# Optimization experiments

Hardware: AMD Instinct MI355X
Metric: run time of the kernel (lower is better)

The kernel has to match this reference:

```python
import jax, jax.numpy as jnp
import numpy as np

FEAT_STRIDE = 16
PRE_NMS, POST_NMS, NMS_THRESH = 6000, 300, 0.7  # state == 'test'

# ---- anchor generation (numpy, done once) ----

def _whctrs(a):
    w = a[2] - a[0] + 1.0
    h = a[3] - a[1] + 1.0
    return w, h, a[0] + 0.5 * (w - 1.0), a[1] + 0.5 * (h - 1.0)

def _mkanchors(ws, hs, xc, yc):
    return np.stack([xc - 0.5 * (ws - 1.0), yc - 0.5 * (hs - 1.0),
                     xc + 0.5 * (ws - 1.0), yc + 0.5 * (hs - 1.0)], axis=1)

def generate_anchors(base_size, scales, ratios):
    base = np.array([0.0, 0.0, base_size - 1.0, base_size - 1.0], np.float64)
    w, h, xc, yc = _whctrs(base)
    size = w * h
    ws = np.round(np.sqrt(size / ratios))
    hs = np.round(ws * ratios)
    ratio_anchors = _mkanchors(ws, hs, xc, yc)
    out = []
    for i in range(ratio_anchors.shape[0]):
        w, h, xc, yc = _whctrs(ratio_anchors[i])
        out.append(_mkanchors(w * scales, h * scales, xc, yc))
    return np.concatenate(out, 0).astype(np.float32)  # [9, 4]

# ---- box utilities ----

def bbox_transform_inv(anchors, deltas):
    widths = anchors[..., 2] - anchors[..., 0] + 1.0
    heights = anchors[..., 3] - anchors[..., 1] + 1.0
    cx = anchors[..., 0] + 0.5 * widths
    cy = anchors[..., 1] + 0.5 * heights
    dx, dy, dw, dh = deltas[..., 0], deltas[..., 1], deltas[..., 2], deltas[..., 3]
    pcx = dx * widths + cx
    pcy = dy * heights + cy
    pw = jnp.exp(dw) * widths
    ph = jnp.exp(dh) * heights
    return jnp.stack([pcx - 0.5 * pw, pcy - 0.5 * ph,
                      pcx + 0.5 * pw, pcy + 0.5 * ph], axis=-1)

def clip_boxes(boxes, img_info):
    # img_info = [height, width]
    x1 = jnp.clip(boxes[..., 0], 0.0, img_info[1] - 1.0)
    y1 = jnp.clip(boxes[..., 1], 0.0, img_info[0] - 1.0)
    x2 = jnp.clip(boxes[..., 2], 0.0, img_info[1] - 1.0)
    y2 = jnp.clip(boxes[..., 3], 0.0, img_info[0] - 1.0)
    return jnp.stack([x1, y1, x2, y2], axis=-1)

def nms_keep(boxes, thresh):
    # boxes [N,4], already sorted by score descending; returns bool keep mask [N]
    n = boxes.shape[0]
    x1, y1, x2, y2 = boxes[:, 0], boxes[:, 1], boxes[:, 2], boxes[:, 3]
    areas = (x2 - x1 + 1.0) * (y2 - y1 + 1.0)
    xx1 = jnp.maximum(x1[:, None], x1[None, :])
    yy1 = jnp.maximum(y1[:, None], y1[None, :])
    xx2 = jnp.minimum(x2[:, None], x2[None, :])
    yy2 = jnp.minimum(y2[:, None], y2[None, :])
    inter = jnp.maximum(0.0, xx2 - xx1 + 1.0) * jnp.maximum(0.0, yy2 - yy1 + 1.0)
    iou = inter / (areas[:, None] + areas[None, :] - inter)  # [N,N]
    over = iou > thresh
    idxs = jnp.arange(n)
    def step(suppressed, i):
        kept = jnp.logical_not(suppressed[i])
        suppressed = suppressed | (kept & over[i] & (idxs > i))
        return suppressed, kept
    _, keep = jax.lax.scan(step, jnp.zeros(n, bool), idxs)
    return keep


def setup_inputs() -> dict:
    key = jax.random.key(0)
    k1, k2 = jax.random.split(key)
    B, H, W = 4, 64, 64
    scores = jax.random.normal(k1, (B, 18, H, W), dtype=jnp.float32)
    bbox_deltas = jax.random.normal(k2, (B, 36, H, W), dtype=jnp.float32)
    img_info = jnp.array([H * FEAT_STRIDE, W * FEAT_STRIDE], dtype=jnp.float32)
    anchors = jnp.asarray(generate_anchors(FEAT_STRIDE,
                                           np.array([8.0, 16.0, 32.0]),
                                           np.array([0.5, 1.0, 2.0])))
    return {"scores": scores, "bbox_deltas": bbox_deltas,
            "img_info": img_info, "anchors": anchors}


def reference(scores, bbox_deltas, img_info, anchors):
    B = scores.shape[0]
    A = anchors.shape[0]
    fg = scores[:, A:]                       # [B, A, H, W] foreground scores
    H, W = fg.shape[2], fg.shape[3]
    sx = jnp.arange(W, dtype=scores.dtype) * FEAT_STRIDE
    sy = jnp.arange(H, dtype=scores.dtype) * FEAT_STRIDE
    gx, gy = jnp.meshgrid(sx, sy)            # 'xy' indexing -> [H, W]
    shifts = jnp.stack([gx.ravel(), gy.ravel(), gx.ravel(), gy.ravel()], -1)  # [K,4]
    all_anchors = (anchors[None] + shifts[:, None]).reshape(-1, 4)            # [K*A,4]
    scs = fg.transpose(0, 2, 3, 1).reshape(B, -1)                # [B, K*A]
    deltas = bbox_deltas.transpose(0, 2, 3, 1).reshape(B, -1, 4)  # [B, K*A, 4]
    props = bbox_transform_inv(all_anchors[None], deltas)
    props = clip_boxes(props, img_info)

    def per_image(args):
        p, s = args
        _, order = jax.lax.top_k(s, PRE_NMS)          # descending score order
        b = p[order]                                   # [PRE_NMS, 4]
        keep = nms_keep(b, NMS_THRESH)
        idx = jnp.where(keep, size=POST_NMS, fill_value=-1)[0]
        valid = (idx >= 0).astype(b.dtype)
        sel = b[jnp.maximum(idx, 0)] * valid[:, None]  # zero-pad missing rows
        return sel                                      # [POST_NMS, 4]

    sel = jax.lax.map(per_image, (props, scs))          # [B, POST_NMS, 4]
    bidx = jnp.broadcast_to(jnp.arange(B, dtype=sel.dtype)[:, None, None],
                            (B, POST_NMS, 1))
    return jnp.concatenate([bidx, sel], axis=-1)        # [B, POST_NMS, 5]
```

## Files before the change

### kernel.cpp

```cpp
#include <hip/hip_runtime.h>
#include <stdint.h>

#define HH 64
#define WW 64
#define AA 9
#define N_PER (HH*WW*AA)
#define NB 4
#define PRE_NMS 6000
#define POST_NMS 300
#define NMS_THRESH 0.7f
#define FEAT_STRIDE 16
#define M 1024
#define MW 16
#define BINS 8192
#define SCAT_MAX 8000

__global__ void __launch_bounds__(1024) select_rank(const float* __restrict__ scores,
                                                    const float* __restrict__ deltas,
                                                    const float* __restrict__ img_info,
                                                    const float* __restrict__ anchors,
                                                    float* __restrict__ topb)
{
#pragma clang fp contract(off)
    int b = blockIdx.x;
    int t = threadIdx.x;
    __shared__ uint32_t H[BINS];
    __shared__ uint32_t SS[BINS];
    __shared__ uint64_t scat[SCAT_MAX];
    __shared__ uint32_t blksum[1024];
    __shared__ int shB1;
    __shared__ uint32_t shNscat;

    auto keyof = [&](int j) -> uint64_t {
        int a = j >> 12, hw = j & 4095;
        float sc = scores[((size_t)b*18 + 9 + a)*4096 + hw];
        uint32_t u = __float_as_uint(sc);
        u = (u & 0x80000000u) ? ~u : (u | 0x80000000u);
        uint32_t i = (uint32_t)(hw*9 + a);
        return ((uint64_t)u << 32) | (uint32_t)(~i);
    };

    for (int i = t; i < BINS; i += 1024) H[i] = 0u;
    __syncthreads();
    for (int j = t; j < N_PER; j += 1024)
        atomicAdd(&H[(uint32_t)(keyof(j) >> 51)], 1u);
    __syncthreads();

    int base = t * 8;
    uint32_t loc[8];
    uint32_t lsum = 0;
    #pragma unroll
    for (int k = 0; k < 8; ++k) { loc[k] = H[base + k]; lsum += loc[k]; }
    blksum[t] = lsum;
    __syncthreads();
    for (int off = 1; off < 1024; off <<= 1) {
        uint32_t add = (t + off < 1024) ? blksum[t + off] : 0u;
        __syncthreads();
        blksum[t] += add;
        __syncthreads();
    }
    uint32_t run = (t < 1023) ? blksum[t + 1] : 0u;
    #pragma unroll
    for (int k = 7; k >= 0; --k) { SS[base + k] = run; run += loc[k]; }
    __syncthreads();

    for (int i = t; i < BINS; i += 1024) {
        if (SS[i] < PRE_NMS && SS[i] + H[i] >= PRE_NMS) shB1 = i;
    }
    __syncthreads();
    int B1 = shB1;
    if (t == 0) shNscat = SS[B1] + H[B1];
    __syncthreads();

    for (int j = t; j < N_PER; j += 1024) {
        uint64_t k64 = keyof(j);
        uint32_t bin = (uint32_t)(k64 >> 51);
        if ((int)bin >= B1) {
            uint32_t slot = atomicAdd(&SS[bin], 1u);
            if (slot < SCAT_MAX) scat[slot] = k64;
        }
    }
    __syncthreads();
    uint32_t Nscat = min(shNscat, (uint32_t)SCAT_MAX);

    float maxx = img_info[1] - 1.0f;
    float maxy = img_info[0] - 1.0f;
    for (uint32_t s = t; s < Nscat; s += 1024) {
        uint64_t k64 = scat[s];
        uint32_t bin = (uint32_t)(k64 >> 51);
        uint32_t end = SS[bin];
        uint32_t start = end - H[bin];
        uint32_t cnt = 0;
        for (uint32_t j = start; j < end; ++j)
            cnt += (scat[j] > k64) ? 1u : 0u;
        uint32_t r = start + cnt;
        if (r < PRE_NMS) {
            uint32_t i = ~(uint32_t)(k64 & 0xFFFFFFFFu);
            int a = (int)(i % 9u);
            int hw = (int)(i / 9u);
            int h = hw >> 6, w = hw & 63;
            float sx = (float)(w * FEAT_STRIDE);
            float sy = (float)(h * FEAT_STRIDE);
            float ax1 = anchors[a*4+0] + sx;
            float ay1 = anchors[a*4+1] + sy;
            float ax2 = anchors[a*4+2] + sx;
            float ay2 = anchors[a*4+3] + sy;
            float width  = ax2 - ax1 + 1.0f;
            float height = ay2 - ay1 + 1.0f;
            float cx = ax1 + 0.5f * width;
            float cy = ay1 + 0.5f * height;
            size_t dbase = ((size_t)b*36 + a*4) * 4096 + hw;
            float dx = deltas[dbase];
            float dy = deltas[dbase + 4096];
            float dw = deltas[dbase + 2*4096];
            float dh = deltas[dbase + 3*4096];
            float pcx = dx * width + cx;
            float pcy = dy * height + cy;
            float pw = (float)exp((double)dw) * width;
            float ph = (float)exp((double)dh) * height;
            float x1 = pcx - 0.5f * pw;
            float y1 = pcy - 0.5f * ph;
            float x2 = pcx + 0.5f * pw;
            float y2 = pcy + 0.5f * ph;
            x1 = fminf(fmaxf(x1, 0.0f), maxx);
            y1 = fminf(fmaxf(y1, 0.0f), maxy);
            x2 = fminf(fmaxf(x2, 0.0f), maxx);
            y2 = fminf(fmaxf(y2, 0.0f), maxy);
            *(float4*)(topb + ((size_t)b*PRE_NMS + r)*4) = make_float4(x1, y1, x2, y2);
        }
    }
}

__global__ void __launch_bounds__(64) nms_mask_small(const float* __restrict__ topb,
                                                     uint64_t* __restrict__ msk) {
#pragma clang fp contract(off)
    int jblock = blockIdx.x;
    int iblock = blockIdx.y;
    int b = blockIdx.z;
    int t = threadIdx.x;
    __shared__ float4 jb[64];
    __shared__ float jarea[64];
    int j0 = jblock*64;
    {
        float4 bj = *(const float4*)(topb + ((size_t)b*PRE_NMS + j0 + t)*4);
        jb[t] = bj;
        jarea[t] = (bj.z - bj.x + 1.0f) * (bj.w - bj.y + 1.0f);
    }
    __syncthreads();
    int i = iblock*64 + t;
    float4 bi = *(const float4*)(topb + ((size_t)b*PRE_NMS + i)*4);
    float areai = (bi.z - bi.x + 1.0f) * (bi.w - bi.y + 1.0f);
    uint64_t bits = 0;
    for (int jj = 0; jj < 64; ++jj) {
        float4 bj = jb[jj];
        float xx1 = fmaxf(bi.x, bj.x);
        float yy1 = fmaxf(bi.y, bj.y);
        float xx2 = fminf(bi.z, bj.z);
        float yy2 = fminf(bi.w, bj.w);
        float iw = fmaxf(0.0f, xx2 - xx1 + 1.0f);
        float ih = fmaxf(0.0f, yy2 - yy1 + 1.0f);
        float inter = iw * ih;
        float iou = inter / ((areai + jarea[jj]) - inter);
        if (iou > NMS_THRESH) bits |= (1ull << jj);
    }
    msk[((size_t)b*M + i)*MW + jblock] = bits;
}

__global__ void __launch_bounds__(64) nms_scan_lds(const uint64_t* __restrict__ msk,
                                                   const float* __restrict__ topb,
                                                   float* __restrict__ out) {
#pragma clang fp contract(off)
    int b = blockIdx.x;
    int l = threadIdx.x;
    __shared__ __align__(16) uint64_t rows[M][MW];
    __shared__ int keepL[POST_NMS];
    __shared__ float skx1[POST_NMS], sky1[POST_NMS], skx2[POST_NMS], sky2[POST_NMS], skar[POST_NMS];

    const uint8_t* src0 = (const uint8_t*)(msk + (size_t)b*M*MW);
    uint8_t* dst0 = (uint8_t*)&rows[0][0];
    for (int it = 0; it < (M*MW*8)/1024; ++it) {
        __builtin_amdgcn_global_load_lds(
            (const __attribute__((address_space(1))) uint32_t*)(src0 + it*1024 + l*16),
            (__attribute__((address_space(3))) uint32_t*)(dst0 + it*1024 + l*16),
            16, 0, 0);
    }
    asm volatile("s_waitcnt vmcnt(0)" ::: "memory");
    __builtin_amdgcn_sched_barrier(0);

    uint64_t remv = 0ull;
    int nkeep = 0;
    int cur = 0;
    bool exhausted = false;
    while (true) {
        if (l == 0) keepL[nkeep] = cur;
        nkeep++;
        if (nkeep >= POST_NMS) break;
        uint64_t rw = (l < MW) ? rows[cur][l] : 0ull;
        remv |= rw;
        uint64_t live = (l < MW) ? ~remv : 0ull;
        int local = live ? (l*64 + (int)__builtin_ctzll(live)) : 0x7FFFFFFF;
        uint64_t mb = __ballot(live != 0ull);
        if (mb == 0ull) { exhausted = true; break; }
        cur = __builtin_amdgcn_readlane(local, (int)__builtin_ctzll(mb));
    }

    if (nkeep < POST_NMS && exhausted) {
        for (int k = l; k < nkeep; k += 64) {
            float4 bx = *(const float4*)(topb + ((size_t)b*PRE_NMS + keepL[k])*4);
            skx1[k] = bx.x; sky1[k] = bx.y; skx2[k] = bx.z; sky2[k] = bx.w;
            skar[k] = (bx.z - bx.x + 1.0f) * (bx.w - bx.y + 1.0f);
        }
        int base = M;
        while (nkeep < POST_NMS && base < PRE_NMS) {
            int c = base + l;
            float4 bc = make_float4(0.f, 0.f, 0.f, 0.f);
            bool sup = true;
            if (c < PRE_NMS) {
                bc = *(const float4*)(topb + ((size_t)b*PRE_NMS + c)*4);
                sup = false;
            }
            float ac = (bc.z - bc.x + 1.0f) * (bc.w - bc.y + 1.0f);
            for (int k = 0; k < nkeep; ++k) {
                float xx1 = fmaxf(skx1[k], bc.x);
                float yy1 = fmaxf(sky1[k], bc.y);
                float xx2 = fminf(skx2[k], bc.z);
                float yy2 = fminf(sky2[k], bc.w);
                float iw = fmaxf(0.0f, xx2 - xx1 + 1.0f);
                float ih = fmaxf(0.0f, yy2 - yy1 + 1.0f);
                float inter = iw * ih;
                float iou = inter / ((skar[k] + ac) - inter);
                if (iou > NMS_THRESH) sup = true;
            }
            uint64_t live = __ballot(!sup);
            while (live != 0ull && nkeep < POST_NMS) {
                int j = (int)__builtin_ctzll(live);
                int cj = base + j;
                if (l == 0) keepL[nkeep] = cj;
                float jx1 = __shfl(bc.x, j);
                float jy1 = __shfl(bc.y, j);
                float jx2 = __shfl(bc.z, j);
                float jy2 = __shfl(bc.w, j);
                float ja  = __shfl(ac, j);
                if (l == 0) { skx1[nkeep]=jx1; sky1[nkeep]=jy1; skx2[nkeep]=jx2; sky2[nkeep]=jy2; skar[nkeep]=ja; }
                nkeep++;
                float xx1 = fmaxf(jx1, bc.x);
                float yy1 = fmaxf(jy1, bc.y);
                float xx2 = fminf(jx2, bc.z);
                float yy2 = fminf(jy2, bc.w);
                float iw = fmaxf(0.0f, xx2 - xx1 + 1.0f);
                float ih = fmaxf(0.0f, yy2 - yy1 + 1.0f);
                float inter = iw * ih;
                float iou = inter / ((ja + ac) - inter);
                uint64_t kill = __ballot(iou > NMS_THRESH);
                live &= ~kill;
                live &= ~(1ull << j);
            }
            base += 64;
        }
    }
    __syncthreads();

    for (int k = l; k < POST_NMS; k += 64) {
        float* o = out + ((size_t)b*POST_NMS + k)*5;
        o[0] = (float)b;
        if (k < nkeep) {
            float4 bx = *(const float4*)(topb + ((size_t)b*PRE_NMS + keepL[k])*4);
            o[1] = bx.x; o[2] = bx.y; o[3] = bx.z; o[4] = bx.w;
        } else {
            o[1] = 0.0f; o[2] = 0.0f; o[3] = 0.0f; o[4] = 0.0f;
        }
    }
}

extern "C" void kernel_launch(void* const* d_in, const int* in_sizes, int n_in,
                              void* d_out, int out_size, void* d_ws, size_t ws_size,
                              hipStream_t stream) {
    const float* scores   = (const float*)d_in[0];
    const float* deltas   = (const float*)d_in[1];
    const float* img_info = (const float*)d_in[2];
    const float* anchors  = (const float*)d_in[3];
    float* out = (float*)d_out;

    uint8_t* ws = (uint8_t*)d_ws;
    float*    topb = (float*)ws;
    uint64_t* msk  = (uint64_t*)(ws + 393216);

    select_rank<<<NB, 1024, 0, stream>>>(scores, deltas, img_info, anchors, topb);

    dim3 mg(MW, MW, NB);
    nms_mask_small<<<mg, 64, 0, stream>>>(topb, msk);

    nms_scan_lds<<<NB, 64, 0, stream>>>(msk, topb, out);
}
```

Measured before the change: 202.4 us.

## Split per-image select/rank kernel into grid-wide histogram, scan, scatter and rank kernels

The single-block-per-image select_rank kernel is replaced by four kernels: a grid-wide global-atomic histogram, a per-image prefix scan and cutoff search, a grid-wide scatter of candidate keys, and a multi-block rank-and-decode pass. The intent is to spread the 36864-element-per-image work across many CUs instead of only four blocks. The cost is extra launches, a memset, global atomics in place of LDS atomics, and intermediates stored in global workspace rather than shared memory.

```diff
diff --git a/kernel.cpp b/kernel.cpp
--- a/kernel.cpp
+++ b/kernel.cpp
@@ -15,42 +15,49 @@
 #define BINS 8192
 #define SCAT_MAX 8000
 
-__global__ void __launch_bounds__(1024) select_rank(const float* __restrict__ scores,
-                                                    const float* __restrict__ deltas,
-                                                    const float* __restrict__ img_info,
-                                                    const float* __restrict__ anchors,
-                                                    float* __restrict__ topb)
-{
-#pragma clang fp contract(off)
+#define OFF_TOPB   0u
+#define OFF_MSK    393216u
+#define OFF_H      917504u
+#define OFF_SS     1048576u
+#define OFF_CUR    1179648u
+#define OFF_B1     1310720u
+#define OFF_NSEL   1310736u
+#define OFF_SCAT   1310752u
+
+__device__ __forceinline__ uint64_t make_key(const float* __restrict__ scores, int b, int j) {
+    int a = j >> 12, hw = j & 4095;
+    float sc = scores[((size_t)b*18 + 9 + a)*4096 + hw];
+    uint32_t u = __float_as_uint(sc);
+    u = (u & 0x80000000u) ? ~u : (u | 0x80000000u);
+    uint32_t i = (uint32_t)(hw*9 + a);
+    return ((uint64_t)u << 32) | (uint32_t)(~i);
+}
+
+__global__ void __launch_bounds__(1024) hist_kernel(const float* __restrict__ scores,
+                                                    uint32_t* __restrict__ Hg) {
+    int tid = blockIdx.x*1024 + threadIdx.x;
+    int b = tid / N_PER;
+    int j = tid - b*N_PER;
+    uint64_t k64 = make_key(scores, b, j);
+    atomicAdd(&Hg[(uint32_t)b*BINS + (uint32_t)(k64 >> 51)], 1u);
+}
+
+__global__ void __launch_bounds__(1024) scan_cutoff(const uint32_t* __restrict__ Hg,
+                                                    uint32_t* __restrict__ SSg,
+                                                    uint32_t* __restrict__ CURg,
+                                                    uint32_t* __restrict__ B1g,
+                                                    uint32_t* __restrict__ NselG) {
     int b = blockIdx.x;
     int t = threadIdx.x;
-    __shared__ uint32_t H[BINS];
     __shared__ uint32_t SS[BINS];
-    __shared__ uint64_t scat[SCAT_MAX];
     __shared__ uint32_t blksum[1024];
     __shared__ int shB1;
-    __shared__ uint32_t shNscat;
-
-    auto keyof = [&](int j) -> uint64_t {
-        int a = j >> 12, hw = j & 4095;
-        float sc = scores[((size_t)b*18 + 9 + a)*4096 + hw];
-        uint32_t u = __float_as_uint(sc);
-        u = (u & 0x80000000u) ? ~u : (u | 0x80000000u);
-        uint32_t i = (uint32_t)(hw*9 + a);
-        return ((uint64_t)u << 32) | (uint32_t)(~i);
-    };
-
-    for (int i = t; i < BINS; i += 1024) H[i] = 0u;
-    __syncthreads();
-    for (int j = t; j < N_PER; j += 1024)
-        atomicAdd(&H[(uint32_t)(keyof(j) >> 51)], 1u);
-    __syncthreads();
 
     int base = t * 8;
     uint32_t loc[8];
     uint32_t lsum = 0;
     #pragma unroll
-    for (int k = 0; k < 8; ++k) { loc[k] = H[base + k]; lsum += loc[k]; }
+    for (int k = 0; k < 8; ++k) { loc[k] = Hg[(uint32_t)b*BINS + base + k]; lsum += loc[k]; }
     blksum[t] = lsum;
     __syncthreads();
     for (int off = 1; off < 1024; off <<= 1) {
@@ -63,72 +70,94 @@
     #pragma unroll
     for (int k = 7; k >= 0; --k) { SS[base + k] = run; run += loc[k]; }
     __syncthreads();
-
-    for (int i = t; i < BINS; i += 1024) {
-        if (SS[i] < PRE_NMS && SS[i] + H[i] >= PRE_NMS) shB1 = i;
-    }
-    __syncthreads();
-    int B1 = shB1;
-    if (t == 0) shNscat = SS[B1] + H[B1];
-    __syncthreads();
-
-    for (int j = t; j < N_PER; j += 1024) {
-        uint64_t k64 = keyof(j);
-        uint32_t bin = (uint32_t)(k64 >> 51);
-        if ((int)bin >= B1) {
-            uint32_t slot = atomicAdd(&SS[bin], 1u);
-            if (slot < SCAT_MAX) scat[slot] = k64;
-        }
-    }
-    __syncthreads();
-    uint32_t Nscat = min(shNscat, (uint32_t)SCAT_MAX);
-
+    #pragma unroll
+    for (int k = 0; k < 8; ++k) {
+        if (SS[base + k] < PRE_NMS && SS[base + k] + loc[k] >= PRE_NMS) shB1 = base + k;
+    }
+    __syncthreads();
+    #pragma unroll
+    for (int k = 0; k < 8; ++k) {
+        SSg[(uint32_t)b*BINS + base + k]  = SS[base + k];
+        CURg[(uint32_t)b*BINS + base + k] = SS[base + k];
+    }
+    if (t == 0) {
+        B1g[b] = (uint32_t)shB1;
+        NselG[b] = SS[shB1] + Hg[(uint32_t)b*BINS + shB1];
+    }
+}
+
+__global__ void __launch_bounds__(1024) scatter_kernel(const float* __restrict__ scores,
+                                                       const uint32_t* __restrict__ B1g,
+                                                       uint32_t* __restrict__ CURg,
+                                                       uint64_t* __restrict__ scatG) {
+    int tid = blockIdx.x*1024 + threadIdx.x;
+    int b = tid / N_PER;
+    int j = tid - b*N_PER;
+    uint64_t k64 = make_key(scores, b, j);
+    uint32_t bin = (uint32_t)(k64 >> 51);
+    if (bin >= B1g[b]) {
+        uint32_t slot = atomicAdd(&CURg[(uint32_t)b*BINS + bin], 1u);
+        if (slot < SCAT_MAX) scatG[(uint32_t)b*SCAT_MAX + slot] = k64;
+    }
+}
+
+__global__ void __launch_bounds__(1024) rank_decode(const uint64_t* __restrict__ scatG,
+                                                    const uint32_t* __restrict__ SSg,
+                                                    const uint32_t* __restrict__ CURg,
+                                                    const uint32_t* __restrict__ NselG,
+                                                    const float* __restrict__ deltas,
+                                                    const float* __restrict__ img_info,
+                                                    const float* __restrict__ anchors,
+                                                    float* __restrict__ topb) {
+#pragma clang fp contract(off)
+    int b = blockIdx.y;
+    uint32_t s = blockIdx.x*1024u + threadIdx.x;
+    uint32_t n = min(NselG[b], (uint32_t)SCAT_MAX);
+    if (s >= n) return;
+    uint64_t k64 = scatG[(uint32_t)b*SCAT_MAX + s];
+    uint32_t bin = (uint32_t)(k64 >> 51);
+    uint32_t start = SSg[(uint32_t)b*BINS + bin];
+    uint32_t end = min(CURg[(uint32_t)b*BINS + bin], (uint32_t)SCAT_MAX);
+    uint32_t cnt = 0;
+    for (uint32_t j = start; j < end; ++j)
+        cnt += (scatG[(uint32_t)b*SCAT_MAX + j] > k64) ? 1u : 0u;
+    uint32_t r = start + cnt;
+    if (r >= PRE_NMS) return;
+
+    uint32_t i = ~(uint32_t)(k64 & 0xFFFFFFFFu);
+    int a = (int)(i % 9u);
+    int hw = (int)(i / 9u);
+    int h = hw >> 6, w = hw & 63;
+    float sx = (float)(w * FEAT_STRIDE);
+    float sy = (float)(h * FEAT_STRIDE);
+    float ax1 = anchors[a*4+0] + sx;
+    float ay1 = anchors[a*4+1] + sy;
+    float ax2 = anchors[a*4+2] + sx;
+    float ay2 = anchors[a*4+3] + sy;
+    float width  = ax2 - ax1 + 1.0f;
+    float height = ay2 - ay1 + 1.0f;
+    float cx = ax1 + 0.5f * width;
+    float cy = ay1 + 0.5f * height;
+    size_t dbase = ((size_t)b*36 + a*4) * 4096 + hw;
+    float dx = deltas[dbase];
+    float dy = deltas[dbase + 4096];
+    float dw = deltas[dbase + 2*4096];
+    float dh = deltas[dbase + 3*4096];
+    float pcx = dx * width + cx;
+    float pcy = dy * height + cy;
+    float pw = (float)exp((double)dw) * width;
+    float ph = (float)exp((double)dh) * height;
+    float x1 = pcx - 0.5f * pw;
+    float y1 = pcy - 0.5f * ph;
+    float x2 = pcx + 0.5f * pw;
+    float y2 = pcy + 0.5f * ph;
     float maxx = img_info[1] - 1.0f;
     float maxy = img_info[0] - 1.0f;
-    for (uint32_t s = t; s < Nscat; s += 1024) {
-        uint64_t k64 = scat[s];
-        uint32_t bin = (uint32_t)(k64 >> 51);
-        uint32_t end = SS[bin];
-        uint32_t start = end - H[bin];
-        uint32_t cnt = 0;
-        for (uint32_t j = start; j < end; ++j)
-            cnt += (scat[j] > k64) ? 1u : 0u;
-        uint32_t r = start + cnt;
-        if (r < PRE_NMS) {
-            uint32_t i = ~(uint32_t)(k64 & 0xFFFFFFFFu);
-            int a = (int)(i % 9u);
-            int hw = (int)(i / 9u);
-            int h = hw >> 6, w = hw & 63;
-            float sx = (float)(w * FEAT_STRIDE);
-            float sy = (float)(h * FEAT_STRIDE);
-            float ax1 = anchors[a*4+0] + sx;
-            float ay1 = anchors[a*4+1] + sy;
-            float ax2 = anchors[a*4+2] + sx;
-            float ay2 = anchors[a*4+3] + sy;
-            float width  = ax2 - ax1 + 1.0f;
-            float height = ay2 - ay1 + 1.0f;
-            float cx = ax1 + 0.5f * width;
-            float cy = ay1 + 0.5f * height;
-            size_t dbase = ((size_t)b*36 + a*4) * 4096 + hw;
-            float dx = deltas[dbase];
-            float dy = deltas[dbase + 4096];
-            float dw = deltas[dbase + 2*4096];
-            float dh = deltas[dbase + 3*4096];
-            float pcx = dx * width + cx;
-            float pcy = dy * height + cy;
-            float pw = (float)exp((double)dw) * width;
-            float ph = (float)exp((double)dh) * height;
-            float x1 = pcx - 0.5f * pw;
-            float y1 = pcy - 0.5f * ph;
-            float x2 = pcx + 0.5f * pw;
-            float y2 = pcy + 0.5f * ph;
-            x1 = fminf(fmaxf(x1, 0.0f), maxx);
-            y1 = fminf(fmaxf(y1, 0.0f), maxy);
-            x2 = fminf(fmaxf(x2, 0.0f), maxx);
-            y2 = fminf(fmaxf(y2, 0.0f), maxy);
-            *(float4*)(topb + ((size_t)b*PRE_NMS + r)*4) = make_float4(x1, y1, x2, y2);
-        }
-    }
+    x1 = fminf(fmaxf(x1, 0.0f), maxx);
+    y1 = fminf(fmaxf(y1, 0.0f), maxy);
+    x2 = fminf(fmaxf(x2, 0.0f), maxx);
+    y2 = fminf(fmaxf(y2, 0.0f), maxy);
+    *(float4*)(topb + ((size_t)b*PRE_NMS + r)*4) = make_float4(x1, y1, x2, y2);
 }
 
 __global__ void __launch_bounds__(64) nms_mask_small(const float* __restrict__ topb,
@@ -282,10 +311,22 @@
     float* out = (float*)d_out;
 
     uint8_t* ws = (uint8_t*)d_ws;
-    float*    topb = (float*)ws;
-    uint64_t* msk  = (uint64_t*)(ws + 393216);
-
-    select_rank<<<NB, 1024, 0, stream>>>(scores, deltas, img_info, anchors, topb);
+    float*    topb  = (float*)(ws + OFF_TOPB);
+    uint64_t* msk   = (uint64_t*)(ws + OFF_MSK);
+    uint32_t* Hg    = (uint32_t*)(ws + OFF_H);
+    uint32_t* SSg   = (uint32_t*)(ws + OFF_SS);
+    uint32_t* CURg  = (uint32_t*)(ws + OFF_CUR);
+    uint32_t* B1g   = (uint32_t*)(ws + OFF_B1);
+    uint32_t* NselG = (uint32_t*)(ws + OFF_NSEL);
+    uint64_t* scatG = (uint64_t*)(ws + OFF_SCAT);
+
+    hipMemsetAsync(Hg, 0, (size_t)NB*BINS*4, stream);
+
+    hist_kernel<<<(NB*N_PER)/1024, 1024, 0, stream>>>(scores, Hg);
+    scan_cutoff<<<NB, 1024, 0, stream>>>(Hg, SSg, CURg, B1g, NselG);
+    scatter_kernel<<<(NB*N_PER)/1024, 1024, 0, stream>>>(scores, B1g, CURg, scatG);
+    rank_decode<<<dim3(SCAT_MAX/1000, NB), 1024, 0, stream>>>(scatG, SSg, CURg, NselG,
+                                                              deltas, img_info, anchors, topb);
 
     dim3 mg(MW, MW, NB);
     nms_mask_small<<<mg, 64, 0, stream>>>(topb, msk);
```

New measurement: 238.8 us. 1.18x slower.
